# Optimization experiments

Measured on AMD Instinct MI355X. Metric: run time of the kernel, lower is better.

## Reference

```python
import jax, jax.numpy as jnp
import numpy as np
import math

PS = 8  # patch size (hard-coded in module)
DEPTH = 6
LAMBDA_INIT = 0.8 - 0.6 * math.exp(-0.3 * DEPTH)

# torch_dct norm=None DCT-II matrix: y_k = 2 * sum_n x_n cos(pi*(2n+1)k/(2N))
_n = np.arange(PS)
_C = 2.0 * np.cos(np.pi * (2 * _n[None, :] + 1) * _n[:, None] / (2 * PS))  # [k, n]
_Ci = np.linalg.inv(_C)
DCT_M = jnp.asarray(_C, jnp.float32)
IDCT_M = jnp.asarray(_Ci, jnp.float32)


def dct2(x):  # 2D DCT over last two dims (torch_dct.dct_2d, norm=None)
    return jnp.einsum('...mn,am,bn->...ab', x, DCT_M, DCT_M)


def idct2(x):  # exact inverse (torch_dct.idct_2d, norm=None)
    return jnp.einsum('...ab,ma,nb->...mn', x, IDCT_M, IDCT_M)


def conv1x1(x, w):  # w: [O, I]
    return jnp.einsum('oi,bihw->bohw', w, x)


def dw3(x, w):  # depthwise 3x3, stride 1, pad 1; w: [C, 1, 3, 3]
    return jax.lax.conv_general_dilated(
        x, w, window_strides=(1, 1), padding='SAME',
        dimension_numbers=('NCHW', 'OIHW', 'NCHW'),
        feature_group_count=x.shape[1])


def prelu(t, a):
    return jnp.where(t >= 0, t, a * t)


def setup_inputs() -> dict:
    key = jax.random.key(0)
    ks = jax.random.split(key, 20)
    b, c, H, W = 2, 64, 384, 384
    w = lambda k, shape: jax.random.normal(k, shape, jnp.float32) * 0.05
    heads = c // 16
    return {
        'x': jax.random.normal(ks[0], (b, c, H, W), jnp.float32),
        'nir': jax.random.normal(ks[1], (b, c, H, W), jnp.float32),
        'w_hidden': w(ks[2], (c, c)),
        'w_hidden_nir': w(ks[3], (2 * c, c)),
        'w_dw': w(ks[4], (c, 1, 3, 3)),
        'w_dw_nir': w(ks[5], (2 * c, 1, 3, 3)),
        'temperature': jnp.ones((heads, 1, 1), jnp.float32),
        'w_proj_mid': w(ks[6], (c, c)),
        'w_proj_out': w(ks[7], (c, c)),
        'w_p1a': w(ks[8], (c, 1, 3, 3)),
        'a_p1': jnp.asarray(0.25, jnp.float32),
        'w_p1b': w(ks[9], (c, 1, 3, 3)),
        'w_p2a': w(ks[10], (c, 1, 3, 3)),
        'a_p2': jnp.asarray(0.25, jnp.float32),
        'w_p2b': w(ks[11], (c, 1, 3, 3)),
        'lq1': jax.random.normal(ks[12], (c,), jnp.float32) * 0.1,
        'lk1': jax.random.normal(ks[13], (c,), jnp.float32) * 0.1,
        'lq2': jax.random.normal(ks[14], (c,), jnp.float32) * 0.1,
        'lk2': jax.random.normal(ks[15], (c,), jnp.float32) * 0.1,
    }


def reference(x, nir, w_hidden, w_hidden_nir, w_dw, w_dw_nir, temperature,
              w_proj_mid, w_proj_out, w_p1a, a_p1, w_p1b, w_p2a, a_p2, w_p2b,
              lq1, lk1, lq2, lk2):
    b, c, H, W = x.shape
    heads = c // 16
    hh, ww = H // PS, W // PS

    hidden = conv1x1(x, w_hidden)
    nir_hidden = conv1x1(nir, w_hidden_nir)
    q = dw3(hidden, w_dw)
    kv = dw3(nir_hidden, w_dw_nir)
    k, v = kv[:, :c], kv[:, c:]

    # b c (hh p1) (ww p2) -> b c hh ww p1 p2
    patch = lambda t: t.reshape(b, c, hh, PS, ww, PS).transpose(0, 1, 2, 4, 3, 5)
    q_fft = dct2(patch(q))
    k_fft = dct2(patch(k))
    out1 = q_fft * k_fft

    L = hh * ww * PS * PS
    hf = lambda t: t.reshape(b, heads, c // heads, L)  # b head c L
    q_fft, k_fft, out1f = hf(q_fft), hf(k_fft), hf(out1)

    qn = q_fft / jnp.maximum(jnp.linalg.norm(q_fft, axis=-1, keepdims=True), 1e-12)
    kn = k_fft / jnp.maximum(jnp.linalg.norm(k_fft, axis=-1, keepdims=True), 1e-12)

    attn = jax.nn.softmax(jnp.einsum('bhcl,bhdl->bhcd', qn, kn) * temperature, axis=-1)
    o = jnp.einsum('bhcd,bhdl->bhcl', attn, out1f)

    o = o.reshape(b, c, hh, ww, PS, PS)
    o = idct2(o)
    o = o.transpose(0, 1, 2, 4, 3, 5).reshape(b, c, H, W)
    out = conv1x1(o, w_proj_mid)

    lam1 = jnp.exp(jnp.sum(lq1 * lk1))
    lam2 = jnp.exp(jnp.sum(lq2 * lk2))
    lam = lam1 - lam2 + LAMBDA_INIT

    pool = lambda t, wa, a, wb: dw3(prelu(dw3(t, wa), a), wb)
    output = pool(q * out, w_p1a, a_p1, w_p1b) + pool(v - lam * (v * out), w_p2a, a_p2, w_p2b)
    return conv1x1(output, w_proj_out)
```

## Files before the change

### kernel.cpp

```cpp
#include <hip/hip_runtime.h>
#include <cmath>

#ifndef M_PI
#define M_PI 3.14159265358979323846
#endif

#define NB      2
#define N_PIX   147456
#define L_LEN   147456
#define TENS_SZ ((long)NB * 64 * N_PIX)

#define OFF_C    0
#define OFF_CI   64
#define OFF_LAM  128
#define OFF_GRAM 256
#define OFF_QQ   2304
#define OFF_KK   2432
#define OFF_ATTN 2560

#define TW 128
#define TH 16
#define LW 136
#define LH 18

__global__ __launch_bounds__(64) void init_k(const float* __restrict__ lq1, const float* __restrict__ lk1,
                                             const float* __restrict__ lq2, const float* __restrict__ lk2,
                                             float* __restrict__ sm) {
  int t = threadIdx.x;
  int a = t >> 3, m = t & 7;
  double cv = 2.0 * cos(M_PI * (double)((2 * m + 1) * a) / 16.0);
  sm[OFF_C + a * 8 + m] = (float)cv;
  sm[OFF_CI + m * 8 + a] = (float)(cv / ((a == 0) ? 32.0 : 16.0));
  float p1 = lq1[t] * lk1[t];
  float p2 = lq2[t] * lk2[t];
  #pragma unroll
  for (int off = 32; off; off >>= 1) {
    p1 += __shfl_xor(p1, off, 64);
    p2 += __shfl_xor(p2, off, 64);
  }
  if (t == 0) sm[OFF_LAM] = expf(p1) - expf(p2) + 0.70082066706704813f;
  for (int i = t; i < 2304; i += 64) sm[OFF_GRAM + i] = 0.f;
}

__global__ void diag_k(float* out, float v) { out[0] = v; }

__global__ __launch_bounds__(256) void conv1x1_k(const float* __restrict__ in, const float* __restrict__ w,
                                                 float* __restrict__ out) {
  __shared__ float ws[4096];
  int t = threadIdx.x;
  for (int j = t; j < 1024; j += 256)
    *reinterpret_cast<float4*>(ws + j * 4) = *reinterpret_cast<const float4*>(w + j * 4);
  __syncthreads();

  long gp = (long)blockIdx.x * 256;
  int bb = (int)(gp / N_PIX);
  int p0 = (int)(gp - (long)bb * N_PIX);
  int lane = t & 63;
  int co0 = (t >> 6) * 16;

  const float* ip = in + (long)bb * 64 * N_PIX + p0 + lane * 4;
  const float* wp = ws + co0 * 64;

  float acc[16][4];
  #pragma unroll
  for (int j = 0; j < 16; j++)
    #pragma unroll
    for (int p = 0; p < 4; p++) acc[j][p] = 0.f;

  for (int c4 = 0; c4 < 16; c4++) {
    float4 x0 = *reinterpret_cast<const float4*>(ip + (long)(c4 * 4 + 0) * N_PIX);
    float4 x1 = *reinterpret_cast<const float4*>(ip + (long)(c4 * 4 + 1) * N_PIX);
    float4 x2 = *reinterpret_cast<const float4*>(ip + (long)(c4 * 4 + 2) * N_PIX);
    float4 x3 = *reinterpret_cast<const float4*>(ip + (long)(c4 * 4 + 3) * N_PIX);
    #pragma unroll
    for (int j = 0; j < 16; j++) {
      float4 w4 = *reinterpret_cast<const float4*>(wp + j * 64 + c4 * 4);
      acc[j][0] = fmaf(w4.x, x0.x, acc[j][0]);
      acc[j][0] = fmaf(w4.y, x1.x, acc[j][0]);
      acc[j][0] = fmaf(w4.z, x2.x, acc[j][0]);
      acc[j][0] = fmaf(w4.w, x3.x, acc[j][0]);
      acc[j][1] = fmaf(w4.x, x0.y, acc[j][1]);
      acc[j][1] = fmaf(w4.y, x1.y, acc[j][1]);
      acc[j][1] = fmaf(w4.z, x2.y, acc[j][1]);
      acc[j][1] = fmaf(w4.w, x3.y, acc[j][1]);
      acc[j][2] = fmaf(w4.x, x0.z, acc[j][2]);
      acc[j][2] = fmaf(w4.y, x1.z, acc[j][2]);
      acc[j][2] = fmaf(w4.z, x2.z, acc[j][2]);
      acc[j][2] = fmaf(w4.w, x3.z, acc[j][2]);
      acc[j][3] = fmaf(w4.x, x0.w, acc[j][3]);
      acc[j][3] = fmaf(w4.y, x1.w, acc[j][3]);
      acc[j][3] = fmaf(w4.z, x2.w, acc[j][3]);
      acc[j][3] = fmaf(w4.w, x3.w, acc[j][3]);
    }
  }

  float* op = out + (long)bb * 64 * N_PIX + p0 + lane * 4;
  #pragma unroll
  for (int j = 0; j < 16; j++)
    *reinterpret_cast<float4*>(op + (long)(co0 + j) * N_PIX) =
        make_float4(acc[j][0], acc[j][1], acc[j][2], acc[j][3]);
}

__device__ __forceinline__ float4 load_g4(const float* __restrict__ p, int gy, int gx) {
  if ((unsigned)gy >= 384u) return make_float4(0.f, 0.f, 0.f, 0.f);
  if (gx >= 0 && gx + 3 < 384) return *reinterpret_cast<const float4*>(p + gy * 384 + gx);
  float e[4];
  #pragma unroll
  for (int i = 0; i < 4; i++) {
    int xx = gx + i;
    e[i] = ((unsigned)xx < 384u) ? p[gy * 384 + xx] : 0.f;
  }
  return make_float4(e[0], e[1], e[2], e[3]);
}

__global__ __launch_bounds__(256) void dw3t_k(const float* __restrict__ in, const float* __restrict__ w,
                                              float* __restrict__ out) {
  __shared__ float sT[LH * LW];
  int plane = blockIdx.z;
  int ch = plane & 63;
  int x0 = blockIdx.x * TW, y0 = blockIdx.y * TH;
  const float* ip = in + (long)plane * N_PIX;
  int t = threadIdx.x;
  for (int j = t; j < LH * 34; j += 256) {
    int row = j / 34, c4 = j - row * 34;
    *reinterpret_cast<float4*>(sT + row * LW + c4 * 4) = load_g4(ip, y0 - 1 + row, x0 - 4 + c4 * 4);
  }
  __syncthreads();
  const float* wp = w + ch * 9;
  float w00 = wp[0], w01 = wp[1], w02 = wp[2];
  float w10 = wp[3], w11 = wp[4], w12 = wp[5];
  float w20 = wp[6], w21 = wp[7], w22 = wp[8];
  int col = t & 127, rg = t >> 7;
  int lc = col + 4;
  int r0 = rg * 8;
  float a0 = sT[r0 * LW + lc - 1],       a1 = sT[r0 * LW + lc],       a2 = sT[r0 * LW + lc + 1];
  float b0 = sT[(r0 + 1) * LW + lc - 1], b1 = sT[(r0 + 1) * LW + lc], b2 = sT[(r0 + 1) * LW + lc + 1];
  float* op = out + (long)plane * N_PIX + (long)(y0 + rg * 8) * 384 + x0 + col;
  #pragma unroll
  for (int i = 0; i < 8; i++) {
    int lr = r0 + i + 2;
    float c0 = sT[lr * LW + lc - 1], c1 = sT[lr * LW + lc], c2 = sT[lr * LW + lc + 1];
    float s = w00 * a0;
    s = fmaf(w01, a1, s); s = fmaf(w02, a2, s);
    s = fmaf(w10, b0, s); s = fmaf(w11, b1, s); s = fmaf(w12, b2, s);
    s = fmaf(w20, c0, s); s = fmaf(w21, c1, s); s = fmaf(w22, c2, s);
    op[i * 384] = s;
    a0 = b0; a1 = b1; a2 = b2;
    b0 = c0; b1 = c1; b2 = c2;
  }
}

__global__ __launch_bounds__(256) void fuseu_k(const float* __restrict__ q, const float* __restrict__ om,
                                               const float* __restrict__ v,
                                               const float* __restrict__ w1a, const float* __restrict__ a1p,
                                               const float* __restrict__ w2a, const float* __restrict__ a2p,
                                               const float* __restrict__ sm,
                                               float* __restrict__ u1, float* __restrict__ u2) {
  __shared__ float s1[LH * LW], s2[LH * LW];
  int plane = blockIdx.z;
  int ch = plane & 63;
  int x0 = blockIdx.x * TW, y0 = blockIdx.y * TH;
  const float* qp = q  + (long)plane * N_PIX;
  const float* op = om + (long)plane * N_PIX;
  const float* vp = v  + (long)plane * N_PIX;
  float lam = sm[OFF_LAM];
  int t = threadIdx.x;
  for (int j = t; j < LH * 34; j += 256) {
    int row = j / 34, c4 = j - row * 34;
    int gy = y0 - 1 + row, gx = x0 - 4 + c4 * 4;
    float4 qv = load_g4(qp, gy, gx);
    float4 ov = load_g4(op, gy, gx);
    float4 vv = load_g4(vp, gy, gx);
    *reinterpret_cast<float4*>(s1 + row * LW + c4 * 4) =
        make_float4(qv.x * ov.x, qv.y * ov.y, qv.z * ov.z, qv.w * ov.w);
    *reinterpret_cast<float4*>(s2 + row * LW + c4 * 4) =
        make_float4(vv.x - lam * vv.x * ov.x, vv.y - lam * vv.y * ov.y,
                    vv.z - lam * vv.z * ov.z, vv.w - lam * vv.w * ov.w);
  }
  __syncthreads();
  const float* wp1 = w1a + ch * 9;
  const float* wp2 = w2a + ch * 9;
  float p00 = wp1[0], p01 = wp1[1], p02 = wp1[2], p10 = wp1[3], p11 = wp1[4], p12 = wp1[5], p20 = wp1[6], p21 = wp1[7], p22 = wp1[8];
  float q00 = wp2[0], q01 = wp2[1], q02 = wp2[2], q10 = wp2[3], q11 = wp2[4], q12 = wp2[5], q20 = wp2[6], q21 = wp2[7], q22 = wp2[8];
  float a1 = a1p[0], a2 = a2p[0];
  int col = t & 127, rg = t >> 7;
  int lc = col + 4;
  int r0 = rg * 8;
  float xa0 = s1[r0 * LW + lc - 1],       xa1 = s1[r0 * LW + lc],       xa2 = s1[r0 * LW + lc + 1];
  float xb0 = s1[(r0 + 1) * LW + lc - 1], xb1 = s1[(r0 + 1) * LW + lc], xb2 = s1[(r0 + 1) * LW + lc + 1];
  float ya0 = s2[r0 * LW + lc - 1],       ya1 = s2[r0 * LW + lc],       ya2 = s2[r0 * LW + lc + 1];
  float yb0 = s2[(r0 + 1) * LW + lc - 1], yb1 = s2[(r0 + 1) * LW + lc], yb2 = s2[(r0 + 1) * LW + lc + 1];
  long obase = (long)plane * N_PIX + (long)(y0 + rg * 8) * 384 + x0 + col;
  #pragma unroll
  for (int i = 0; i < 8; i++) {
    int lr = r0 + i + 2;
    float xc0 = s1[lr * LW + lc - 1], xc1 = s1[lr * LW + lc], xc2 = s1[lr * LW + lc + 1];
    float yc0 = s2[lr * LW + lc - 1], yc1 = s2[lr * LW + lc], yc2 = s2[lr * LW + lc + 1];
    float su = p00 * xa0;
    su = fmaf(p01, xa1, su); su = fmaf(p02, xa2, su);
    su = fmaf(p10, xb0, su); su = fmaf(p11, xb1, su); su = fmaf(p12, xb2, su);
    su = fmaf(p20, xc0, su); su = fmaf(p21, xc1, su); su = fmaf(p22, xc2, su);
    float sv = q00 * ya0;
    sv = fmaf(q01, ya1, sv); sv = fmaf(q02, ya2, sv);
    sv = fmaf(q10, yb0, sv); sv = fmaf(q11, yb1, sv); sv = fmaf(q12, yb2, sv);
    sv = fmaf(q20, yc0, sv); sv = fmaf(q21, yc1, sv); sv = fmaf(q22, yc2, sv);
    u1[obase + i * 384] = (su >= 0.f) ? su : a1 * su;
    u2[obase + i * 384] = (sv >= 0.f) ? sv : a2 * sv;
    xa0 = xb0; xa1 = xb1; xa2 = xb2; xb0 = xc0; xb1 = xc1; xb2 = xc2;
    ya0 = yb0; ya1 = yb1; ya2 = yb2; yb0 = yc0; yb1 = yc1; yb2 = yc2;
  }
}

__global__ __launch_bounds__(256) void dw3dual_k(const float* __restrict__ u1, const float* __restrict__ u2,
                                                 const float* __restrict__ w1b, const float* __restrict__ w2b,
                                                 float* __restrict__ out) {
  __shared__ float s1[LH * LW], s2[LH * LW];
  int plane = blockIdx.z;
  int ch = plane & 63;
  int x0 = blockIdx.x * TW, y0 = blockIdx.y * TH;
  const float* p1 = u1 + (long)plane * N_PIX;
  const float* p2 = u2 + (long)plane * N_PIX;
  int t = threadIdx.x;
  for (int j = t; j < LH * 34; j += 256) {
    int row = j / 34, c4 = j - row * 34;
    int gy = y0 - 1 + row, gx = x0 - 4 + c4 * 4;
    *reinterpret_cast<float4*>(s1 + row * LW + c4 * 4) = load_g4(p1, gy, gx);
    *reinterpret_cast<float4*>(s2 + row * LW + c4 * 4) = load_g4(p2, gy, gx);
  }
  __syncthreads();
  const float* wp1 = w1b + ch * 9;
  const float* wp2 = w2b + ch * 9;
  float p00 = wp1[0], p01 = wp1[1], p02 = wp1[2], p10 = wp1[3], p11 = wp1[4], p12 = wp1[5], p20 = wp1[6], p21 = wp1[7], p22 = wp1[8];
  float q00 = wp2[0], q01 = wp2[1], q02 = wp2[2], q10 = wp2[3], q11 = wp2[4], q12 = wp2[5], q20 = wp2[6], q21 = wp2[7], q22 = wp2[8];
  int col = t & 127, rg = t >> 7;
  int lc = col + 4;
  int r0 = rg * 8;
  float xa0 = s1[r0 * LW + lc - 1],       xa1 = s1[r0 * LW + lc],       xa2 = s1[r0 * LW + lc + 1];
  float xb0 = s1[(r0 + 1) * LW + lc - 1], xb1 = s1[(r0 + 1) * LW + lc], xb2 = s1[(r0 + 1) * LW + lc + 1];
  float ya0 = s2[r0 * LW + lc - 1],       ya1 = s2[r0 * LW + lc],       ya2 = s2[r0 * LW + lc + 1];
  float yb0 = s2[(r0 + 1) * LW + lc - 1], yb1 = s2[(r0 + 1) * LW + lc], yb2 = s2[(r0 + 1) * LW + lc + 1];
  float* op = out + (long)plane * N_PIX + (long)(y0 + rg * 8) * 384 + x0 + col;
  #pragma unroll
  for (int i = 0; i < 8; i++) {
    int lr = r0 + i + 2;
    float xc0 = s1[lr * LW + lc - 1], xc1 = s1[lr * LW + lc], xc2 = s1[lr * LW + lc + 1];
    float yc0 = s2[lr * LW + lc - 1], yc1 = s2[lr * LW + lc], yc2 = s2[lr * LW + lc + 1];
    float s = p00 * xa0;
    s = fmaf(p01, xa1, s); s = fmaf(p02, xa2, s);
    s = fmaf(p10, xb0, s); s = fmaf(p11, xb1, s); s = fmaf(p12, xb2, s);
    s = fmaf(p20, xc0, s); s = fmaf(p21, xc1, s); s = fmaf(p22, xc2, s);
    s = fmaf(q00, ya0, s); s = fmaf(q01, ya1, s); s = fmaf(q02, ya2, s);
    s = fmaf(q10, yb0, s); s = fmaf(q11, yb1, s); s = fmaf(q12, yb2, s);
    s = fmaf(q20, yc0, s); s = fmaf(q21, yc1, s); s = fmaf(q22, yc2, s);
    op[i * 384] = s;
    xa0 = xb0; xa1 = xb1; xa2 = xb2; xb0 = xc0; xb1 = xc1; xb2 = xc2;
    ya0 = yb0; ya1 = yb1; ya2 = yb2; yb0 = yc0; yb1 = yc1; yb2 = yc2;
  }
}

__global__ __launch_bounds__(256) void dct_k(const float* __restrict__ in,
                                             const float* __restrict__ sm, float* __restrict__ outf) {
  __shared__ float Cm[64];
  if (threadIdx.x < 64) Cm[threadIdx.x] = sm[OFF_C + threadIdx.x];
  __syncthreads();
  int pid = blockIdx.x * 256 + threadIdx.x;
  int wx = pid % 48;
  int t1 = pid / 48;
  int hy = t1 % 48; t1 /= 48;
  int ch = t1 & 63;
  int bb = t1 >> 6;
  const float* ip = in + (long)(bb * 64 + ch) * N_PIX + (hy * 8) * 384 + wx * 8;
  float X[8][8];
  #pragma unroll
  for (int r = 0; r < 8; r++) {
    float4 v0 = *reinterpret_cast<const float4*>(ip + r * 384);
    float4 v1 = *reinterpret_cast<const float4*>(ip + r * 384 + 4);
    X[r][0] = v0.x; X[r][1] = v0.y; X[r][2] = v0.z; X[r][3] = v0.w;
    X[r][4] = v1.x; X[r][5] = v1.y; X[r][6] = v1.z; X[r][7] = v1.w;
  }
  float T[8][8];
  #pragma unroll
  for (int a = 0; a < 8; a++)
    #pragma unroll
    for (int n = 0; n < 8; n++) {
      float s = 0.f;
      #pragma unroll
      for (int m = 0; m < 8; m++) s = fmaf(Cm[a * 8 + m], X[m][n], s);
      T[a][n] = s;
    }
  #pragma unroll
  for (int a = 0; a < 8; a++)
    #pragma unroll
    for (int b8 = 0; b8 < 8; b8++) {
      float s = 0.f;
      #pragma unroll
      for (int n = 0; n < 8; n++) s = fmaf(Cm[b8 * 8 + n], T[a][n], s);
      X[a][b8] = s;
    }
  float* op = outf + (long)(bb * 64 + ch) * L_LEN + (long)(hy * 48 + wx) * 64;
  float4* o4 = reinterpret_cast<float4*>(op);
  #pragma unroll
  for (int a = 0; a < 8; a++) {
    o4[a * 2]     = make_float4(X[a][0], X[a][1], X[a][2], X[a][3]);
    o4[a * 2 + 1] = make_float4(X[a][4], X[a][5], X[a][6], X[a][7]);
  }
}

#define GS_P 132
__global__ __launch_bounds__(256) void gram_k(const float* __restrict__ qf, const float* __restrict__ kf,
                                              float* __restrict__ sm) {
  __shared__ float qs[16 * GS_P], ks[16 * GS_P];
  int t = threadIdx.x;
  int bh = blockIdx.y;
  int bb = bh >> 2, h = bh & 3;
  const float* qbase = qf + ((long)bb * 64 + h * 16) * L_LEN;
  const float* kbase = kf + ((long)bb * 64 + h * 16) * L_LEN;
  int c = t >> 4, d = t & 15;
  long l0 = (long)blockIdx.x * 2048;
  float g = 0.f, nq = 0.f, nk = 0.f;
  for (int chunk = 0; chunk < 16; chunk++) {
    long lc = l0 + chunk * 128;
    __syncthreads();
    for (int j = t; j < 512; j += 256) {
      int row = j >> 5, c4 = j & 31;
      *reinterpret_cast<float4*>(qs + row * GS_P + c4 * 4) =
          *reinterpret_cast<const float4*>(qbase + (long)row * L_LEN + lc + c4 * 4);
      *reinterpret_cast<float4*>(ks + row * GS_P + c4 * 4) =
          *reinterpret_cast<const float4*>(kbase + (long)row * L_LEN + lc + c4 * 4);
    }
    __syncthreads();
    #pragma unroll
    for (int i = 0; i < 128; i += 4) {
      float4 a = *reinterpret_cast<const float4*>(qs + c * GS_P + i);
      float4 b = *reinterpret_cast<const float4*>(ks + d * GS_P + i);
      g  = fmaf(a.x, b.x, g);  g  = fmaf(a.y, b.y, g);  g  = fmaf(a.z, b.z, g);  g  = fmaf(a.w, b.w, g);
      nq = fmaf(a.x, a.x, nq); nq = fmaf(a.y, a.y, nq); nq = fmaf(a.z, a.z, nq); nq = fmaf(a.w, a.w, nq);
      nk = fmaf(b.x, b.x, nk); nk = fmaf(b.y, b.y, nk); nk = fmaf(b.z, b.z, nk); nk = fmaf(b.w, b.w, nk);
    }
  }
  atomicAdd(&sm[OFF_GRAM + bh * 256 + c * 16 + d], g);
  if (d == 0) atomicAdd(&sm[OFF_QQ + bh * 16 + c], nq);
  if (c == 0) atomicAdd(&sm[OFF_KK + bh * 16 + d], nk);
}

__global__ __launch_bounds__(256) void attn_k(const float* __restrict__ temp, float* __restrict__ sm) {
  int bh = blockIdx.x;
  int h = bh & 3;
  int t = threadIdx.x;
  int c = t >> 4, d = t & 15;
  float qn = fmaxf(sqrtf(sm[OFF_QQ + bh * 16 + c]), 1e-12f);
  float kn = fmaxf(sqrtf(sm[OFF_KK + bh * 16 + d]), 1e-12f);
  float v = sm[OFF_GRAM + bh * 256 + t] / (qn * kn) * temp[h];
  float mx = v;
  #pragma unroll
  for (int o = 8; o; o >>= 1) mx = fmaxf(mx, __shfl_xor(mx, o, 16));
  float e = expf(v - mx);
  float s = e;
  #pragma unroll
  for (int o = 8; o; o >>= 1) s += __shfl_xor(s, o, 16);
  sm[OFF_ATTN + bh * 256 + t] = e / s;
}

__global__ __launch_bounds__(256) void combine_k(float* __restrict__ qf, const float* __restrict__ kf,
                                                 const float* __restrict__ sm) {
  __shared__ float A[256];
  int bh = blockIdx.y;
  A[threadIdx.x] = sm[OFF_ATTN + bh * 256 + threadIdx.x];
  __syncthreads();
  int bb = bh >> 2, h = bh & 3;
  long l = (long)blockIdx.x * 256 + threadIdx.x;
  float* qp = qf + ((long)bb * 64 + h * 16) * L_LEN + l;
  const float* kp = kf + ((long)bb * 64 + h * 16) * L_LEN + l;
  float p[16];
  #pragma unroll
  for (int d = 0; d < 16; d++) p[d] = qp[(long)d * L_LEN] * kp[(long)d * L_LEN];
  #pragma unroll
  for (int c = 0; c < 16; c++) {
    float s = 0.f;
    #pragma unroll
    for (int d = 0; d < 16; d++) s = fmaf(A[c * 16 + d], p[d], s);
    qp[(long)c * L_LEN] = s;
  }
}

__global__ __launch_bounds__(256) void idct_k(const float* __restrict__ inf, const float* __restrict__ sm,
                                              float* __restrict__ out) {
  __shared__ float Ci[64];
  if (threadIdx.x < 64) Ci[threadIdx.x] = sm[OFF_CI + threadIdx.x];
  __syncthreads();
  int pid = blockIdx.x * 256 + threadIdx.x;
  int wx = pid % 48;
  int t1 = pid / 48;
  int hy = t1 % 48; t1 /= 48;
  int ch = t1 & 63;
  int bb = t1 >> 6;
  const float4* i4 = reinterpret_cast<const float4*>(inf + (long)(bb * 64 + ch) * L_LEN + (long)(hy * 48 + wx) * 64);
  float F[8][8];
  #pragma unroll
  for (int a = 0; a < 8; a++) {
    float4 v0 = i4[a * 2], v1 = i4[a * 2 + 1];
    F[a][0] = v0.x; F[a][1] = v0.y; F[a][2] = v0.z; F[a][3] = v0.w;
    F[a][4] = v1.x; F[a][5] = v1.y; F[a][6] = v1.z; F[a][7] = v1.w;
  }
  float T[8][8];
  #pragma unroll
  for (int m = 0; m < 8; m++)
    #pragma unroll
    for (int b8 = 0; b8 < 8; b8++) {
      float s = 0.f;
      #pragma unroll
      for (int a = 0; a < 8; a++) s = fmaf(Ci[m * 8 + a], F[a][b8], s);
      T[m][b8] = s;
    }
  #pragma unroll
  for (int m = 0; m < 8; m++)
    #pragma unroll
    for (int n = 0; n < 8; n++) {
      float s = 0.f;
      #pragma unroll
      for (int b8 = 0; b8 < 8; b8++) s = fmaf(Ci[n * 8 + b8], T[m][b8], s);
      F[m][n] = s;
    }
  float* op = out + (long)(bb * 64 + ch) * N_PIX + (hy * 8) * 384 + wx * 8;
  #pragma unroll
  for (int m = 0; m < 8; m++) {
    *reinterpret_cast<float4*>(op + m * 384)     = make_float4(F[m][0], F[m][1], F[m][2], F[m][3]);
    *reinterpret_cast<float4*>(op + m * 384 + 4) = make_float4(F[m][4], F[m][5], F[m][6], F[m][7]);
  }
}

extern "C" void kernel_launch(void* const* d_in, const int* in_sizes, int n_in,
                              void* d_out, int out_size, void* d_ws, size_t ws_size,
                              hipStream_t stream) {
  const float* x            = (const float*)d_in[0];
  const float* nir          = (const float*)d_in[1];
  const float* w_hidden     = (const float*)d_in[2];
  const float* w_hidden_nir = (const float*)d_in[3];
  const float* w_dw         = (const float*)d_in[4];
  const float* w_dw_nir     = (const float*)d_in[5];
  const float* temperature  = (const float*)d_in[6];
  const float* w_proj_mid   = (const float*)d_in[7];
  const float* w_proj_out   = (const float*)d_in[8];
  const float* w_p1a        = (const float*)d_in[9];
  const float* a_p1         = (const float*)d_in[10];
  const float* w_p1b        = (const float*)d_in[11];
  const float* w_p2a        = (const float*)d_in[12];
  const float* a_p2         = (const float*)d_in[13];
  const float* w_p2b        = (const float*)d_in[14];
  const float* lq1          = (const float*)d_in[15];
  const float* lk1          = (const float*)d_in[16];
  const float* lq2          = (const float*)d_in[17];
  const float* lk2          = (const float*)d_in[18];

  float* OUT = (float*)d_out;
  float* W0 = (float*)d_ws;
  float* W1 = W0 + TENS_SZ;
  float* W2 = W1 + TENS_SZ;
  float* SM = W2 + TENS_SZ;

  size_t needed = (size_t)3 * TENS_SZ * sizeof(float) + 32768;
  if (ws_size < needed) {
    diag_k<<<1, 1, 0, stream>>>(OUT, 1000.0f + (float)(ws_size >> 20));
    return;
  }

  dim3 blk256(256);
  dim3 gridST(3, 24, NB * 64);

  init_k<<<1, 64, 0, stream>>>(lq1, lk1, lq2, lk2, SM);
  conv1x1_k<<<1152, blk256, 0, stream>>>(x, w_hidden, W0);
  dw3t_k<<<gridST, blk256, 0, stream>>>(W0, w_dw, OUT);
  conv1x1_k<<<1152, blk256, 0, stream>>>(nir, w_hidden_nir, W0);
  dw3t_k<<<gridST, blk256, 0, stream>>>(W0, w_dw_nir, W1);
  conv1x1_k<<<1152, blk256, 0, stream>>>(nir, w_hidden_nir + 64 * 64, W0);
  dw3t_k<<<gridST, blk256, 0, stream>>>(W0, w_dw_nir + 64 * 9, W2);
  dct_k<<<1152, blk256, 0, stream>>>(W1, SM, W0);
  dct_k<<<1152, blk256, 0, stream>>>(OUT, SM, W1);
  gram_k<<<dim3(72, 8), blk256, 0, stream>>>(W1, W0, SM);
  attn_k<<<8, blk256, 0, stream>>>(temperature, SM);
  combine_k<<<dim3(576, 8), blk256, 0, stream>>>(W1, W0, SM);
  idct_k<<<1152, blk256, 0, stream>>>(W1, SM, W0);
  conv1x1_k<<<1152, blk256, 0, stream>>>(W0, w_proj_mid, W1);
  fuseu_k<<<gridST, blk256, 0, stream>>>(OUT, W1, W2, w_p1a, a_p1, w_p2a, a_p2, SM, W0, OUT);
  dw3dual_k<<<gridST, blk256, 0, stream>>>(W0, OUT, w_p1b, w_p2b, W1);
  conv1x1_k<<<1152, blk256, 0, stream>>>(W1, w_proj_out, OUT);
}
```

Baseline: 807.8 us.

## Fuse attention combine with IDCT and fuse both pooling depthwise stages

Adds a comb_idct kernel that applies the attention matrix and then does the inverse 8x8 DCT through shared memory. It writes spatial output to a fourth workspace buffer when the workspace is large enough, and falls back to the old combine and idct path otherwise. The two pooling depthwise-conv stages are also merged into one kernel that keeps the PReLU intermediate in shared memory with a halo recompute. This removes two full-tensor write and read round trips, at the cost of more shared memory per block, which may lower occupancy.

```diff
diff --git a/kernel.cpp b/kernel.cpp
--- a/kernel.cpp
+++ b/kernel.cpp
@@ -22,6 +22,8 @@
 #define TH 16
 #define LW 136
 #define LH 18
+#define PLH 20
+#define PIH 18
 
 __global__ __launch_bounds__(64) void init_k(const float* __restrict__ lq1, const float* __restrict__ lk1,
                                              const float* __restrict__ lq2, const float* __restrict__ lk2,
@@ -150,13 +152,16 @@
   }
 }
 
-__global__ __launch_bounds__(256) void fuseu_k(const float* __restrict__ q, const float* __restrict__ om,
-                                               const float* __restrict__ v,
-                                               const float* __restrict__ w1a, const float* __restrict__ a1p,
-                                               const float* __restrict__ w2a, const float* __restrict__ a2p,
-                                               const float* __restrict__ sm,
-                                               float* __restrict__ u1, float* __restrict__ u2) {
-  __shared__ float s1[LH * LW], s2[LH * LW];
+__global__ __launch_bounds__(256) void pool_k(const float* __restrict__ q, const float* __restrict__ om,
+                                              const float* __restrict__ v,
+                                              const float* __restrict__ w1a, const float* __restrict__ a1p,
+                                              const float* __restrict__ w1b,
+                                              const float* __restrict__ w2a, const float* __restrict__ a2p,
+                                              const float* __restrict__ w2b,
+                                              const float* __restrict__ sm,
+                                              float* __restrict__ outp) {
+  __shared__ float s1[PLH * LW], s2[PLH * LW];
+  __shared__ float i1[PIH * LW], i2[PIH * LW];
   int plane = blockIdx.z;
   int ch = plane & 63;
   int x0 = blockIdx.x * TW, y0 = blockIdx.y * TH;
@@ -165,9 +170,9 @@
   const float* vp = v  + (long)plane * N_PIX;
   float lam = sm[OFF_LAM];
   int t = threadIdx.x;
-  for (int j = t; j < LH * 34; j += 256) {
+  for (int j = t; j < PLH * 34; j += 256) {
     int row = j / 34, c4 = j - row * 34;
-    int gy = y0 - 1 + row, gx = x0 - 4 + c4 * 4;
+    int gy = y0 - 2 + row, gx = x0 - 4 + c4 * 4;
     float4 qv = load_g4(qp, gy, gx);
     float4 ov = load_g4(op, gy, gx);
     float4 vv = load_g4(vp, gy, gx);
@@ -178,83 +183,80 @@
                     vv.z - lam * vv.z * ov.z, vv.w - lam * vv.w * ov.w);
   }
   __syncthreads();
-  const float* wp1 = w1a + ch * 9;
-  const float* wp2 = w2a + ch * 9;
-  float p00 = wp1[0], p01 = wp1[1], p02 = wp1[2], p10 = wp1[3], p11 = wp1[4], p12 = wp1[5], p20 = wp1[6], p21 = wp1[7], p22 = wp1[8];
-  float q00 = wp2[0], q01 = wp2[1], q02 = wp2[2], q10 = wp2[3], q11 = wp2[4], q12 = wp2[5], q20 = wp2[6], q21 = wp2[7], q22 = wp2[8];
-  float a1 = a1p[0], a2 = a2p[0];
-  int col = t & 127, rg = t >> 7;
-  int lc = col + 4;
-  int r0 = rg * 8;
-  float xa0 = s1[r0 * LW + lc - 1],       xa1 = s1[r0 * LW + lc],       xa2 = s1[r0 * LW + lc + 1];
-  float xb0 = s1[(r0 + 1) * LW + lc - 1], xb1 = s1[(r0 + 1) * LW + lc], xb2 = s1[(r0 + 1) * LW + lc + 1];
-  float ya0 = s2[r0 * LW + lc - 1],       ya1 = s2[r0 * LW + lc],       ya2 = s2[r0 * LW + lc + 1];
-  float yb0 = s2[(r0 + 1) * LW + lc - 1], yb1 = s2[(r0 + 1) * LW + lc], yb2 = s2[(r0 + 1) * LW + lc + 1];
-  long obase = (long)plane * N_PIX + (long)(y0 + rg * 8) * 384 + x0 + col;
-  #pragma unroll
-  for (int i = 0; i < 8; i++) {
-    int lr = r0 + i + 2;
-    float xc0 = s1[lr * LW + lc - 1], xc1 = s1[lr * LW + lc], xc2 = s1[lr * LW + lc + 1];
-    float yc0 = s2[lr * LW + lc - 1], yc1 = s2[lr * LW + lc], yc2 = s2[lr * LW + lc + 1];
-    float su = p00 * xa0;
-    su = fmaf(p01, xa1, su); su = fmaf(p02, xa2, su);
-    su = fmaf(p10, xb0, su); su = fmaf(p11, xb1, su); su = fmaf(p12, xb2, su);
-    su = fmaf(p20, xc0, su); su = fmaf(p21, xc1, su); su = fmaf(p22, xc2, su);
-    float sv = q00 * ya0;
-    sv = fmaf(q01, ya1, sv); sv = fmaf(q02, ya2, sv);
-    sv = fmaf(q10, yb0, sv); sv = fmaf(q11, yb1, sv); sv = fmaf(q12, yb2, sv);
-    sv = fmaf(q20, yc0, sv); sv = fmaf(q21, yc1, sv); sv = fmaf(q22, yc2, sv);
-    u1[obase + i * 384] = (su >= 0.f) ? su : a1 * su;
-    u2[obase + i * 384] = (sv >= 0.f) ? sv : a2 * sv;
-    xa0 = xb0; xa1 = xb1; xa2 = xb2; xb0 = xc0; xb1 = xc1; xb2 = xc2;
-    ya0 = yb0; ya1 = yb1; ya2 = yb2; yb0 = yc0; yb1 = yc1; yb2 = yc2;
-  }
-}
-
-__global__ __launch_bounds__(256) void dw3dual_k(const float* __restrict__ u1, const float* __restrict__ u2,
-                                                 const float* __restrict__ w1b, const float* __restrict__ w2b,
-                                                 float* __restrict__ out) {
-  __shared__ float s1[LH * LW], s2[LH * LW];
-  int plane = blockIdx.z;
-  int ch = plane & 63;
-  int x0 = blockIdx.x * TW, y0 = blockIdx.y * TH;
-  const float* p1 = u1 + (long)plane * N_PIX;
-  const float* p2 = u2 + (long)plane * N_PIX;
-  int t = threadIdx.x;
-  for (int j = t; j < LH * 34; j += 256) {
-    int row = j / 34, c4 = j - row * 34;
-    int gy = y0 - 1 + row, gx = x0 - 4 + c4 * 4;
-    *reinterpret_cast<float4*>(s1 + row * LW + c4 * 4) = load_g4(p1, gy, gx);
-    *reinterpret_cast<float4*>(s2 + row * LW + c4 * 4) = load_g4(p2, gy, gx);
-  }
-  __syncthreads();
-  const float* wp1 = w1b + ch * 9;
-  const float* wp2 = w2b + ch * 9;
-  float p00 = wp1[0], p01 = wp1[1], p02 = wp1[2], p10 = wp1[3], p11 = wp1[4], p12 = wp1[5], p20 = wp1[6], p21 = wp1[7], p22 = wp1[8];
-  float q00 = wp2[0], q01 = wp2[1], q02 = wp2[2], q10 = wp2[3], q11 = wp2[4], q12 = wp2[5], q20 = wp2[6], q21 = wp2[7], q22 = wp2[8];
-  int col = t & 127, rg = t >> 7;
-  int lc = col + 4;
-  int r0 = rg * 8;
-  float xa0 = s1[r0 * LW + lc - 1],       xa1 = s1[r0 * LW + lc],       xa2 = s1[r0 * LW + lc + 1];
-  float xb0 = s1[(r0 + 1) * LW + lc - 1], xb1 = s1[(r0 + 1) * LW + lc], xb2 = s1[(r0 + 1) * LW + lc + 1];
-  float ya0 = s2[r0 * LW + lc - 1],       ya1 = s2[r0 * LW + lc],       ya2 = s2[r0 * LW + lc + 1];
-  float yb0 = s2[(r0 + 1) * LW + lc - 1], yb1 = s2[(r0 + 1) * LW + lc], yb2 = s2[(r0 + 1) * LW + lc + 1];
-  float* op = out + (long)plane * N_PIX + (long)(y0 + rg * 8) * 384 + x0 + col;
-  #pragma unroll
-  for (int i = 0; i < 8; i++) {
-    int lr = r0 + i + 2;
-    float xc0 = s1[lr * LW + lc - 1], xc1 = s1[lr * LW + lc], xc2 = s1[lr * LW + lc + 1];
-    float yc0 = s2[lr * LW + lc - 1], yc1 = s2[lr * LW + lc], yc2 = s2[lr * LW + lc + 1];
-    float s = p00 * xa0;
-    s = fmaf(p01, xa1, s); s = fmaf(p02, xa2, s);
-    s = fmaf(p10, xb0, s); s = fmaf(p11, xb1, s); s = fmaf(p12, xb2, s);
-    s = fmaf(p20, xc0, s); s = fmaf(p21, xc1, s); s = fmaf(p22, xc2, s);
-    s = fmaf(q00, ya0, s); s = fmaf(q01, ya1, s); s = fmaf(q02, ya2, s);
-    s = fmaf(q10, yb0, s); s = fmaf(q11, yb1, s); s = fmaf(q12, yb2, s);
-    s = fmaf(q20, yc0, s); s = fmaf(q21, yc1, s); s = fmaf(q22, yc2, s);
-    op[i * 384] = s;
-    xa0 = xb0; xa1 = xb1; xa2 = xb2; xb0 = xc0; xb1 = xc1; xb2 = xc2;
-    ya0 = yb0; ya1 = yb1; ya2 = yb2; yb0 = yc0; yb1 = yc1; yb2 = yc2;
+  {
+    const float* wp1 = w1a + ch * 9;
+    const float* wp2 = w2a + ch * 9;
+    float p00 = wp1[0], p01 = wp1[1], p02 = wp1[2], p10 = wp1[3], p11 = wp1[4], p12 = wp1[5], p20 = wp1[6], p21 = wp1[7], p22 = wp1[8];
+    float q00 = wp2[0], q01 = wp2[1], q02 = wp2[2], q10 = wp2[3], q11 = wp2[4], q12 = wp2[5], q20 = wp2[6], q21 = wp2[7], q22 = wp2[8];
+    float a1 = a1p[0], a2 = a2p[0];
+    int ct = t & 127, rg = t >> 7;
+    #pragma unroll
+    for (int pass = 0; pass < 2; pass++) {
+      int ci = 3 + ct + pass * 128;
+      if (ci <= 132) {
+        int gx = x0 - 4 + ci;
+        bool xok = (unsigned)gx < 384u;
+        int rs0 = rg * 9;
+        float xa0 = s1[rs0 * LW + ci - 1],       xa1 = s1[rs0 * LW + ci],       xa2 = s1[rs0 * LW + ci + 1];
+        float xb0 = s1[(rs0 + 1) * LW + ci - 1], xb1 = s1[(rs0 + 1) * LW + ci], xb2 = s1[(rs0 + 1) * LW + ci + 1];
+        float ya0 = s2[rs0 * LW + ci - 1],       ya1 = s2[rs0 * LW + ci],       ya2 = s2[rs0 * LW + ci + 1];
+        float yb0 = s2[(rs0 + 1) * LW + ci - 1], yb1 = s2[(rs0 + 1) * LW + ci], yb2 = s2[(rs0 + 1) * LW + ci + 1];
+        #pragma unroll
+        for (int ii = 0; ii < 9; ii++) {
+          int rs2 = rs0 + ii + 2;
+          float xc0 = s1[rs2 * LW + ci - 1], xc1 = s1[rs2 * LW + ci], xc2 = s1[rs2 * LW + ci + 1];
+          float yc0 = s2[rs2 * LW + ci - 1], yc1 = s2[rs2 * LW + ci], yc2 = s2[rs2 * LW + ci + 1];
+          float su = p00 * xa0;
+          su = fmaf(p01, xa1, su); su = fmaf(p02, xa2, su);
+          su = fmaf(p10, xb0, su); su = fmaf(p11, xb1, su); su = fmaf(p12, xb2, su);
+          su = fmaf(p20, xc0, su); su = fmaf(p21, xc1, su); su = fmaf(p22, xc2, su);
+          float sv = q00 * ya0;
+          sv = fmaf(q01, ya1, sv); sv = fmaf(q02, ya2, sv);
+          sv = fmaf(q10, yb0, sv); sv = fmaf(q11, yb1, sv); sv = fmaf(q12, yb2, sv);
+          sv = fmaf(q20, yc0, sv); sv = fmaf(q21, yc1, sv); sv = fmaf(q22, yc2, sv);
+          su = (su >= 0.f) ? su : a1 * su;
+          sv = (sv >= 0.f) ? sv : a2 * sv;
+          int ri = rs0 + ii;
+          int gy = y0 - 1 + ri;
+          bool ok = xok && ((unsigned)gy < 384u);
+          i1[ri * LW + ci] = ok ? su : 0.f;
+          i2[ri * LW + ci] = ok ? sv : 0.f;
+          xa0 = xb0; xa1 = xb1; xa2 = xb2; xb0 = xc0; xb1 = xc1; xb2 = xc2;
+          ya0 = yb0; ya1 = yb1; ya2 = yb2; yb0 = yc0; yb1 = yc1; yb2 = yc2;
+        }
+      }
+    }
+  }
+  __syncthreads();
+  {
+    const float* wp1 = w1b + ch * 9;
+    const float* wp2 = w2b + ch * 9;
+    float p00 = wp1[0], p01 = wp1[1], p02 = wp1[2], p10 = wp1[3], p11 = wp1[4], p12 = wp1[5], p20 = wp1[6], p21 = wp1[7], p22 = wp1[8];
+    float q00 = wp2[0], q01 = wp2[1], q02 = wp2[2], q10 = wp2[3], q11 = wp2[4], q12 = wp2[5], q20 = wp2[6], q21 = wp2[7], q22 = wp2[8];
+    int col = t & 127, rg = t >> 7;
+    int lc = col + 4;
+    int r0 = rg * 8;
+    float xa0 = i1[r0 * LW + lc - 1],       xa1 = i1[r0 * LW + lc],       xa2 = i1[r0 * LW + lc + 1];
+    float xb0 = i1[(r0 + 1) * LW + lc - 1], xb1 = i1[(r0 + 1) * LW + lc], xb2 = i1[(r0 + 1) * LW + lc + 1];
+    float ya0 = i2[r0 * LW + lc - 1],       ya1 = i2[r0 * LW + lc],       ya2 = i2[r0 * LW + lc + 1];
+    float yb0 = i2[(r0 + 1) * LW + lc - 1], yb1 = i2[(r0 + 1) * LW + lc], yb2 = i2[(r0 + 1) * LW + lc + 1];
+    float* wo = outp + (long)plane * N_PIX + (long)(y0 + rg * 8) * 384 + x0 + col;
+    #pragma unroll
+    for (int i = 0; i < 8; i++) {
+      int lr = r0 + i + 2;
+      float xc0 = i1[lr * LW + lc - 1], xc1 = i1[lr * LW + lc], xc2 = i1[lr * LW + lc + 1];
+      float yc0 = i2[lr * LW + lc - 1], yc1 = i2[lr * LW + lc], yc2 = i2[lr * LW + lc + 1];
+      float s = p00 * xa0;
+      s = fmaf(p01, xa1, s); s = fmaf(p02, xa2, s);
+      s = fmaf(p10, xb0, s); s = fmaf(p11, xb1, s); s = fmaf(p12, xb2, s);
+      s = fmaf(p20, xc0, s); s = fmaf(p21, xc1, s); s = fmaf(p22, xc2, s);
+      s = fmaf(q00, ya0, s); s = fmaf(q01, ya1, s); s = fmaf(q02, ya2, s);
+      s = fmaf(q10, yb0, s); s = fmaf(q11, yb1, s); s = fmaf(q12, yb2, s);
+      s = fmaf(q20, yc0, s); s = fmaf(q21, yc1, s); s = fmaf(q22, yc2, s);
+      wo[i * 384] = s;
+      xa0 = xb0; xa1 = xb1; xa2 = xb2; xb0 = xc0; xb1 = xc1; xb2 = xc2;
+      ya0 = yb0; ya1 = yb1; ya2 = yb2; yb0 = yc0; yb1 = yc1; yb2 = yc2;
+    }
   }
 }
 
@@ -359,6 +361,66 @@
   #pragma unroll
   for (int o = 8; o; o >>= 1) s += __shfl_xor(s, o, 16);
   sm[OFF_ATTN + bh * 256 + t] = e / s;
+}
+
+#define CB_P 260
+__global__ __launch_bounds__(256) void comb_idct_k(const float* __restrict__ qf, const float* __restrict__ kf,
+                                                   const float* __restrict__ sm, float* __restrict__ out) {
+  __shared__ float A[256];
+  __shared__ float Ci[64];
+  __shared__ float sb[16 * CB_P];
+  int bh = blockIdx.y;
+  int t = threadIdx.x;
+  A[t] = sm[OFF_ATTN + bh * 256 + t];
+  if (t < 64) Ci[t] = sm[OFF_CI + t];
+  __syncthreads();
+  int bb = bh >> 2, h = bh & 3;
+  long l = (long)blockIdx.x * 256 + t;
+  const float* qp = qf + ((long)bb * 64 + h * 16) * L_LEN + l;
+  const float* kp = kf + ((long)bb * 64 + h * 16) * L_LEN + l;
+  float p[16];
+  #pragma unroll
+  for (int d = 0; d < 16; d++) p[d] = qp[(long)d * L_LEN] * kp[(long)d * L_LEN];
+  #pragma unroll
+  for (int c = 0; c < 16; c++) {
+    float s = 0.f;
+    #pragma unroll
+    for (int d = 0; d < 16; d++) s = fmaf(A[c * 16 + d], p[d], s);
+    sb[c * CB_P + t] = s;
+  }
+  __syncthreads();
+  int j = t & 3, c = (t >> 2) & 15, pl = t >> 6;
+  const float* fb = sb + c * CB_P + pl * 64;
+  float F[8][8];
+  #pragma unroll
+  for (int a = 0; a < 8; a++)
+    #pragma unroll
+    for (int b8 = 0; b8 < 8; b8++) F[a][b8] = fb[a * 8 + b8];
+  int patch = blockIdx.x * 4 + pl;
+  int hy = patch / 48, wx = patch - hy * 48;
+  float* op = out + ((long)bb * 64 + h * 16 + c) * N_PIX + (long)(hy * 8) * 384 + wx * 8;
+  #pragma unroll
+  for (int mm = 0; mm < 2; mm++) {
+    int m = 2 * j + mm;
+    float T[8];
+    #pragma unroll
+    for (int b8 = 0; b8 < 8; b8++) {
+      float s = 0.f;
+      #pragma unroll
+      for (int a = 0; a < 8; a++) s = fmaf(Ci[m * 8 + a], F[a][b8], s);
+      T[b8] = s;
+    }
+    float o[8];
+    #pragma unroll
+    for (int n = 0; n < 8; n++) {
+      float s = 0.f;
+      #pragma unroll
+      for (int b8 = 0; b8 < 8; b8++) s = fmaf(Ci[n * 8 + b8], T[b8], s);
+      o[n] = s;
+    }
+    *reinterpret_cast<float4*>(op + m * 384)     = make_float4(o[0], o[1], o[2], o[3]);
+    *reinterpret_cast<float4*>(op + m * 384 + 4) = make_float4(o[4], o[5], o[6], o[7]);
+  }
 }
 
 __global__ __launch_bounds__(256) void combine_k(float* __restrict__ qf, const float* __restrict__ kf,
@@ -457,12 +519,15 @@
   float* W1 = W0 + TENS_SZ;
   float* W2 = W1 + TENS_SZ;
   float* SM = W2 + TENS_SZ;
-
-  size_t needed = (size_t)3 * TENS_SZ * sizeof(float) + 32768;
-  if (ws_size < needed) {
+  float* W3 = SM + 8192;
+
+  size_t needed3 = (size_t)3 * TENS_SZ * sizeof(float) + 32768;
+  size_t needed4 = ((size_t)4 * TENS_SZ + 8192) * sizeof(float);
+  if (ws_size < needed3) {
     diag_k<<<1, 1, 0, stream>>>(OUT, 1000.0f + (float)(ws_size >> 20));
     return;
   }
+  bool big = ws_size >= needed4;
 
   dim3 blk256(256);
   dim3 gridST(3, 24, NB * 64);
@@ -478,10 +543,17 @@
   dct_k<<<1152, blk256, 0, stream>>>(OUT, SM, W1);
   gram_k<<<dim3(72, 8), blk256, 0, stream>>>(W1, W0, SM);
   attn_k<<<8, blk256, 0, stream>>>(temperature, SM);
-  combine_k<<<dim3(576, 8), blk256, 0, stream>>>(W1, W0, SM);
-  idct_k<<<1152, blk256, 0, stream>>>(W1, SM, W0);
-  conv1x1_k<<<1152, blk256, 0, stream>>>(W0, w_proj_mid, W1);
-  fuseu_k<<<gridST, blk256, 0, stream>>>(OUT, W1, W2, w_p1a, a_p1, w_p2a, a_p2, SM, W0, OUT);
-  dw3dual_k<<<gridST, blk256, 0, stream>>>(W0, OUT, w_p1b, w_p2b, W1);
-  conv1x1_k<<<1152, blk256, 0, stream>>>(W1, w_proj_out, OUT);
-}
+
+  float* o_spatial;
+  if (big) {
+    comb_idct_k<<<dim3(576, 8), blk256, 0, stream>>>(W1, W0, SM, W3);
+    o_spatial = W3;
+  } else {
+    combine_k<<<dim3(576, 8), blk256, 0, stream>>>(W1, W0, SM);
+    idct_k<<<1152, blk256, 0, stream>>>(W1, SM, W0);
+    o_spatial = W0;
+  }
+  conv1x1_k<<<1152, blk256, 0, stream>>>(o_spatial, w_proj_mid, W1);
+  pool_k<<<gridST, blk256, 0, stream>>>(OUT, W1, W2, w_p1a, a_p1, w_p1b, w_p2a, a_p2, w_p2b, SM, W0);
+  conv1x1_k<<<1152, blk256, 0, stream>>>(W0, w_proj_out, OUT);
+}
```

After: 811.7 us. About the same (+0.5%).
